# Optimization experiments

Hardware: AMD Instinct MI355X
Metric: run time of the kernel (lower is better)

Reference implementation:

```python
import jax, jax.numpy as jnp
import numpy as np

IN_F, OUT_F, RANK = 4096, 4096, 16
SCALING = 1.0  # alpha defaults to rank -> alpha/rank == 1.0


def setup_inputs() -> dict:
    key = jax.random.key(0)
    k1, k2, k3, k4 = jax.random.split(key, 4)
    x = jax.random.normal(k1, (4, 2048, IN_F), dtype=jnp.float32)
    base_weight = jax.random.normal(k2, (OUT_F, IN_F), dtype=jnp.float32)
    U = jax.random.normal(k3, (OUT_F, RANK), dtype=jnp.float32)
    s = jnp.ones((RANK,), dtype=jnp.float32)
    V = jax.random.normal(k4, (IN_F, RANK), dtype=jnp.float32)
    return {"x": x, "base_weight": base_weight, "U": U, "s": s, "V": V}


def reference(x, base_weight, U, s, V):
    # delta_weight = scaling * (U * s) @ V^T, shape (out, in)
    delta_w = SCALING * jnp.einsum('or,ir->oi', U * s[None, :], V)
    adapted = base_weight + delta_w
    # x @ adapted^T : (..., in) -> (..., out)
    return jnp.einsum('bsi,oi->bso', x, adapted)
```

## Files before the change

### kernel.cpp

```cpp
#include <hip/hip_runtime.h>


#define IN_F   4096
#define OUT_F  4096
#define RANK   16
#define M_ROWS 8192
#define BM 256
#define BN 256
#define BK 64
#define NT (IN_F / BK)

typedef _Float16 f16x8 __attribute__((ext_vector_type(8)));
typedef _Float16 f16x4 __attribute__((ext_vector_type(4)));
typedef float    f32x4 __attribute__((ext_vector_type(4)));

__device__ __forceinline__ void async16(const void* gp, void* lp) {
  __builtin_amdgcn_global_load_lds(
      (const __attribute__((address_space(1))) void*)gp,
      (__attribute__((address_space(3))) void*)lp, 16, 0, 0);
}

#define SPLIT_BLOCKS 4096

__global__ __launch_bounds__(256)
void prep_kernel(const float* __restrict__ x, _Float16* __restrict__ xh,
                 const float* __restrict__ W, const float* __restrict__ U,
                 const float* __restrict__ S, const float* __restrict__ V,
                 _Float16* __restrict__ wh) {
  if (blockIdx.x < SPLIT_BLOCKS) {
    size_t t = (size_t)blockIdx.x * 256 + threadIdx.x;
#pragma unroll
    for (int it = 0; it < 8; ++it) {
      float4 v = ((const float4*)x)[t];
      f16x4 h;
      h[0] = (_Float16)v.x; h[1] = (_Float16)v.y;
      h[2] = (_Float16)v.z; h[3] = (_Float16)v.w;
      ((f16x4*)xh)[t] = h;
      t += (size_t)SPLIT_BLOCKS * 256;
    }
  } else {
    int t = (int)(blockIdx.x - SPLIT_BLOCKS) * 256 + threadIdx.x;
    int i4 = (t & 1023) << 2;
    int o0 = (t >> 10) << 3;

    float v[4][RANK];
#pragma unroll
    for (int j = 0; j < 4; ++j) {
      const float4* vp = (const float4*)(V + (size_t)(i4 + j) * RANK);
#pragma unroll
      for (int q = 0; q < 4; ++q) {
        float4 vv = vp[q];
        v[j][q * 4 + 0] = vv.x; v[j][q * 4 + 1] = vv.y;
        v[j][q * 4 + 2] = vv.z; v[j][q * 4 + 3] = vv.w;
      }
    }
    float sv[RANK];
#pragma unroll
    for (int r = 0; r < RANK; r += 4) {
      float4 ss = *(const float4*)(S + r);
      sv[r] = ss.x; sv[r + 1] = ss.y; sv[r + 2] = ss.z; sv[r + 3] = ss.w;
    }

    for (int oo = 0; oo < 8; ++oo) {
      int o = o0 + oo;
      float us[RANK];
      const float4* up = (const float4*)(U + (size_t)o * RANK);
#pragma unroll
      for (int r = 0; r < RANK; r += 4) {
        float4 uu = up[r >> 2];
        us[r] = uu.x * sv[r]; us[r + 1] = uu.y * sv[r + 1];
        us[r + 2] = uu.z * sv[r + 2]; us[r + 3] = uu.w * sv[r + 3];
      }
      float4 w = *(const float4*)(W + (size_t)o * IN_F + i4);
      float d0 = w.x, d1 = w.y, d2 = w.z, d3 = w.w;
#pragma unroll
      for (int r = 0; r < RANK; ++r) {
        d0 += us[r] * v[0][r];
        d1 += us[r] * v[1][r];
        d2 += us[r] * v[2][r];
        d3 += us[r] * v[3][r];
      }
      f16x4 h;
      h[0] = (_Float16)d0; h[1] = (_Float16)d1;
      h[2] = (_Float16)d2; h[3] = (_Float16)d3;
      *(f16x4*)(wh + (size_t)o * IN_F + i4) = h;
    }
  }
}

__global__ __launch_bounds__(512, 2)
void gemm_kernel(const _Float16* __restrict__ xh,
                 const _Float16* __restrict__ wh,
                 float* __restrict__ out) {
  __shared__ unsigned char lds[131072];

  const int orig = blockIdx.x;
  const int wg = (orig & 7) * 64 + (orig >> 3);
  const int mt = wg >> 4;
  const int nt = wg & 15;
  const int blockM = mt * BM;
  const int blockN = nt * BN;

  const int tid = threadIdx.x;
  const int lane = tid & 63;
  const int wave = tid >> 6;
  const int wm = wave >> 2;
  const int wn = wave & 3;

  const _Float16* aSrc[2];
  const _Float16* bSrc[2];
  unsigned ldsOff[2];
#pragma unroll
  for (int q = 0; q < 2; ++q) {
    int slot = q * 512 + tid;
    int r = slot >> 2;
    int c = slot & 3;
    int cd = c ^ ((r >> 1) & 3);
    aSrc[q] = xh + (size_t)(blockM + r) * IN_F + cd * 8;
    bSrc[q] = wh + (size_t)(blockN + r) * IN_F + cd * 8;
    ldsOff[q] = (unsigned)slot * 16;
  }

  const int kg = lane >> 4;
  unsigned offA[4], offB[4];
#pragma unroll
  for (int t = 0; t < 4; ++t) {
    int ar = wm * 128 + t * 16 + (lane & 15);
    offA[t] = (unsigned)(ar * 64 + ((kg ^ ((ar >> 1) & 3)) * 16));
    int br = wn * 64 + t * 16 + (lane & 15);
    offB[t] = (unsigned)(br * 64 + ((kg ^ ((br >> 1) & 3)) * 16));
  }

  f32x4 acc[8][4];
#pragma unroll
  for (int i = 0; i < 8; ++i)
#pragma unroll
    for (int j = 0; j < 4; ++j) acc[i][j] = (f32x4){0.f, 0.f, 0.f, 0.f};

  f16x8 aFA[4], aFB[4], bF0[4], bF1[4];

#define STG(SRC, LDSBASE, KOFS)                                      \
  {                                                                  \
    async16(SRC[0] + (KOFS), lds + (LDSBASE) + ldsOff[0]);           \
    async16(SRC[1] + (KOFS), lds + (LDSBASE) + ldsOff[1]);           \
  }
#define RD4(DST, RB, OFF)                                            \
  {                                                                  \
    DST[0] = *(const f16x8*)(lds + (RB) + OFF[0]);                   \
    DST[1] = *(const f16x8*)(lds + (RB) + OFF[1]);                   \
    DST[2] = *(const f16x8*)(lds + (RB) + OFF[2]);                   \
    DST[3] = *(const f16x8*)(lds + (RB) + OFF[3]);                   \
  }
#define PH_BAR() asm volatile("s_barrier" ::: "memory")
#define WAITL(N) asm volatile("s_waitcnt lgkmcnt(" #N ")" ::: "memory")
#define WAITV(N) asm volatile("s_waitcnt vmcnt(" #N ")" ::: "memory")
#define MFMA16(AO, A, B)                                             \
  {                                                                  \
    __builtin_amdgcn_sched_barrier(0);                               \
    __builtin_amdgcn_s_setprio(1);                                   \
    _Pragma("unroll")                                                \
    for (int i_ = 0; i_ < 4; ++i_) {                                 \
      _Pragma("unroll")                                              \
      for (int j_ = 0; j_ < 4; ++j_)                                 \
        acc[(AO) + i_][j_] = __builtin_amdgcn_mfma_f32_16x16x32_f16( \
            (A)[i_], (B)[j_], acc[(AO) + i_][j_], 0, 0, 0);          \
    }                                                                \
    __builtin_amdgcn_s_setprio(0);                                   \
  }

  STG(aSrc, 0, 0);
  STG(bSrc, 16384, 0);
  STG(aSrc, 32768, 32);
  STG(bSrc, 49152, 32);
  STG(bSrc, 65536 + 16384, 64);
  STG(aSrc, 65536 + 0, 64);
  STG(bSrc, 65536 + 49152, 96);
  WAITV(6);
  PH_BAR();
  RD4(aFA, 0, offA);
  RD4(bF0, 16384, offB);

#pragma unroll 2
  for (int t = 0; t < NT - 2; ++t) {
    const unsigned base  = (unsigned)(t & 1) << 16;
    const unsigned baseN = base ^ 65536u;
    const int kof1 = (t + 1) * BK;
    const int kof2 = (t + 2) * BK;

    PH_BAR();
    RD4(aFB, base + 4096, offA);
    STG(aSrc, baseN + 32768, kof1 + 32);
    WAITL(4);
    MFMA16(0, aFA, bF0);

    PH_BAR();
    RD4(aFA, base + 32768, offA);
    RD4(bF1, base + 49152, offB);
    STG(bSrc, base + 16384, kof2);
    WAITL(8);
    MFMA16(4, aFB, bF0);

    PH_BAR();
    RD4(aFB, base + 32768 + 4096, offA);
    STG(aSrc, base + 0, kof2);
    WAITL(4);
    MFMA16(0, aFA, bF1);

    WAITV(4);
    PH_BAR();
    RD4(aFA, baseN + 0, offA);
    RD4(bF0, baseN + 16384, offB);
    STG(bSrc, base + 49152, kof2 + 32);
    WAITL(8);
    MFMA16(4, aFB, bF1);
  }

  {
    const unsigned base = 0, baseN = 65536u;
    const int kof1 = (NT - 1) * BK;
    PH_BAR();
    RD4(aFB, base + 4096, offA);
    STG(aSrc, baseN + 32768, kof1 + 32);
    WAITL(4);
    MFMA16(0, aFA, bF0);

    PH_BAR();
    RD4(aFA, base + 32768, offA);
    RD4(bF1, base + 49152, offB);
    WAITL(8);
    MFMA16(4, aFB, bF0);

    PH_BAR();
    RD4(aFB, base + 32768 + 4096, offA);
    WAITL(4);
    MFMA16(0, aFA, bF1);

    WAITV(0);
    PH_BAR();
    RD4(aFA, baseN + 0, offA);
    RD4(bF0, baseN + 16384, offB);
    WAITL(8);
    MFMA16(4, aFB, bF1);
  }
  {
    const unsigned base = 65536u;
    PH_BAR();
    RD4(aFB, base + 4096, offA);
    WAITL(4);
    MFMA16(0, aFA, bF0);

    PH_BAR();
    RD4(aFA, base + 32768, offA);
    RD4(bF1, base + 49152, offB);
    WAITL(8);
    MFMA16(4, aFB, bF0);

    PH_BAR();
    RD4(aFB, base + 32768 + 4096, offA);
    WAITL(4);
    MFMA16(0, aFA, bF1);

    PH_BAR();
    WAITL(0);
    MFMA16(4, aFB, bF1);
  }
#undef STG
#undef RD4
#undef PH_BAR
#undef WAITL
#undef WAITV
#undef MFMA16

  const int col0 = blockN + wn * 64 + (lane & 15);
  const int row0 = blockM + wm * 128 + (lane >> 4) * 4;
#pragma unroll
  for (int i = 0; i < 8; ++i)
#pragma unroll
    for (int j = 0; j < 4; ++j) {
      float* op = out + (size_t)(row0 + i * 16) * OUT_F + col0 + j * 16;
#pragma unroll
      for (int rr = 0; rr < 4; ++rr) op[(size_t)rr * OUT_F] = acc[i][j][rr];
    }
}

__global__ __launch_bounds__(256)
void fb_gemm(const float* __restrict__ x, const float* __restrict__ W,
             float* __restrict__ out) {
  __shared__ float xs[64][17];
  __shared__ float wsm[64][17];
  const int mt = blockIdx.x >> 6;
  const int ntile = blockIdx.x & 63;
  const int bM = mt * 64, bN = ntile * 64;
  const int t = threadIdx.x;
  const int lr = t >> 2, lc = (t & 3) * 4;
  const int tm = t >> 4, tn = t & 15;

  float acc[4][4];
#pragma unroll
  for (int i = 0; i < 4; ++i)
#pragma unroll
    for (int j = 0; j < 4; ++j) acc[i][j] = 0.f;

  for (int kk = 0; kk < IN_F; kk += 16) {
    float4 xa = *(const float4*)(x + (size_t)(bM + lr) * IN_F + kk + lc);
    float4 wa = *(const float4*)(W + (size_t)(bN + lr) * IN_F + kk + lc);
    xs[lr][lc + 0] = xa.x; xs[lr][lc + 1] = xa.y;
    xs[lr][lc + 2] = xa.z; xs[lr][lc + 3] = xa.w;
    wsm[lr][lc + 0] = wa.x; wsm[lr][lc + 1] = wa.y;
    wsm[lr][lc + 2] = wa.z; wsm[lr][lc + 3] = wa.w;
    __syncthreads();
#pragma unroll
    for (int k = 0; k < 16; ++k) {
      float a[4], b[4];
#pragma unroll
      for (int i = 0; i < 4; ++i) a[i] = xs[tm * 4 + i][k];
#pragma unroll
      for (int j = 0; j < 4; ++j) b[j] = wsm[tn * 4 + j][k];
#pragma unroll
      for (int i = 0; i < 4; ++i)
#pragma unroll
        for (int j = 0; j < 4; ++j) acc[i][j] += a[i] * b[j];
    }
    __syncthreads();
  }
#pragma unroll
  for (int i = 0; i < 4; ++i)
#pragma unroll
    for (int j = 0; j < 4; ++j)
      out[(size_t)(bM + tm * 4 + i) * OUT_F + bN + tn * 4 + j] = acc[i][j];
}

__global__ void fb_xv(const float* __restrict__ x, const float* __restrict__ V,
                      const float* __restrict__ S, float* __restrict__ xv) {
  int m = blockIdx.x * 4 + (threadIdx.x >> 6);
  int lane = threadIdx.x & 63;
  float a[RANK];
#pragma unroll
  for (int r = 0; r < RANK; ++r) a[r] = 0.f;
  for (int k = lane; k < IN_F; k += 64) {
    float xe = x[(size_t)m * IN_F + k];
    const float4* vp = (const float4*)(V + (size_t)k * RANK);
#pragma unroll
    for (int q = 0; q < 4; ++q) {
      float4 vv = vp[q];
      a[q * 4 + 0] += xe * vv.x; a[q * 4 + 1] += xe * vv.y;
      a[q * 4 + 2] += xe * vv.z; a[q * 4 + 3] += xe * vv.w;
    }
  }
#pragma unroll
  for (int r = 0; r < RANK; ++r)
    for (int off = 32; off; off >>= 1) a[r] += __shfl_down(a[r], off);
  if (lane == 0) {
#pragma unroll
    for (int r = 0; r < RANK; ++r) xv[(size_t)m * RANK + r] = a[r] * S[r];
  }
}

__global__ void fb_add(const float* __restrict__ xv, const float* __restrict__ U,
                       float* __restrict__ out) {
  size_t t = (size_t)blockIdx.x * 256 + threadIdx.x;
  int m = (int)(t >> 12), o = (int)(t & 4095);
  const float* xr = xv + (size_t)m * RANK;
  const float* ur = U + (size_t)o * RANK;
  float d = 0.f;
#pragma unroll
  for (int r = 0; r < RANK; ++r) d += xr[r] * ur[r];
  out[t] += d;
}

extern "C" void kernel_launch(void* const* d_in, const int* in_sizes, int n_in,
                              void* d_out, int out_size, void* d_ws, size_t ws_size,
                              hipStream_t stream) {
  const float* x = (const float*)d_in[0];
  const float* W = (const float*)d_in[1];
  const float* U = (const float*)d_in[2];
  const float* s = (const float*)d_in[3];
  const float* V = (const float*)d_in[4];
  float* out = (float*)d_out;

  const size_t need = ((size_t)M_ROWS * IN_F + (size_t)OUT_F * IN_F) * 2;
  if (ws_size >= need) {
    _Float16* xh = (_Float16*)d_ws;
    _Float16* wh = xh + (size_t)M_ROWS * IN_F;
    prep_kernel<<<SPLIT_BLOCKS + ((IN_F / 4) * (OUT_F / 8)) / 256, 256, 0, stream>>>(
        x, xh, W, U, s, V, wh);
    gemm_kernel<<<(M_ROWS / BM) * (OUT_F / BN), 512, 0, stream>>>(xh, wh, out);
  } else {
    float* xv = (float*)d_ws;
    fb_gemm<<<(M_ROWS / 64) * (OUT_F / 64), 256, 0, stream>>>(x, W, out);
    fb_xv<<<M_ROWS / 4, 256, 0, stream>>>(x, V, s, xv);
    fb_add<<<(size_t)M_ROWS * OUT_F / 256, 256, 0, stream>>>(xv, U, out);
  }
}
```

Before: 537.9 us.

## Switch main GEMM to 32x32x16 MFMA tiles and widen fp16 conversion stores

Replaces the 16x16x32 MFMA inner tiling with 32x32x16 MFMA instructions. This changes the per-lane LDS fragment offsets, the accumulator layout (f32x16), the LDS read schedule and wait counts, the staging order, and the output write mapping. Larger MFMA tiles reduce LDS fragment reads per FLOP and the instruction count. The prep kernel also converts x with 8-wide fp16 stores instead of 4-wide. The trade-off is reworked pipeline wait counts, which risk hazards or stalls, and a less coalesced epilogue store pattern.

Result: no change. 538.5 us (+0.1%).

```diff
diff --git a/kernel.cpp b/kernel.cpp
--- a/kernel.cpp
+++ b/kernel.cpp
@@ -13,6 +13,7 @@
 typedef _Float16 f16x8 __attribute__((ext_vector_type(8)));
 typedef _Float16 f16x4 __attribute__((ext_vector_type(4)));
 typedef float    f32x4 __attribute__((ext_vector_type(4)));
+typedef float    f32x16 __attribute__((ext_vector_type(16)));
 
 __device__ __forceinline__ void async16(const void* gp, void* lp) {
   __builtin_amdgcn_global_load_lds(
@@ -29,13 +30,17 @@
                  _Float16* __restrict__ wh) {
   if (blockIdx.x < SPLIT_BLOCKS) {
     size_t t = (size_t)blockIdx.x * 256 + threadIdx.x;
-#pragma unroll
-    for (int it = 0; it < 8; ++it) {
-      float4 v = ((const float4*)x)[t];
-      f16x4 h;
-      h[0] = (_Float16)v.x; h[1] = (_Float16)v.y;
-      h[2] = (_Float16)v.z; h[3] = (_Float16)v.w;
-      ((f16x4*)xh)[t] = h;
+    const float4* xin = (const float4*)x;
+#pragma unroll
+    for (int it = 0; it < 4; ++it) {
+      float4 a = xin[2 * t];
+      float4 b = xin[2 * t + 1];
+      f16x8 h;
+      h[0] = (_Float16)a.x; h[1] = (_Float16)a.y;
+      h[2] = (_Float16)a.z; h[3] = (_Float16)a.w;
+      h[4] = (_Float16)b.x; h[5] = (_Float16)b.y;
+      h[6] = (_Float16)b.z; h[7] = (_Float16)b.w;
+      ((f16x8*)xh)[t] = h;
       t += (size_t)SPLIT_BLOCKS * 256;
     }
   } else {
@@ -121,49 +126,59 @@
     ldsOff[q] = (unsigned)slot * 16;
   }
 
-  const int kg = lane >> 4;
-  unsigned offA[4], offB[4];
-#pragma unroll
-  for (int t = 0; t < 4; ++t) {
-    int ar = wm * 128 + t * 16 + (lane & 15);
-    offA[t] = (unsigned)(ar * 64 + ((kg ^ ((ar >> 1) & 3)) * 16));
-    int br = wn * 64 + t * 16 + (lane & 15);
-    offB[t] = (unsigned)(br * 64 + ((kg ^ ((br >> 1) & 3)) * 16));
-  }
-
-  f32x4 acc[8][4];
-#pragma unroll
-  for (int i = 0; i < 8; ++i)
-#pragma unroll
-    for (int j = 0; j < 4; ++j) acc[i][j] = (f32x4){0.f, 0.f, 0.f, 0.f};
-
-  f16x8 aFA[4], aFB[4], bF0[4], bF1[4];
+  const int kg = lane >> 5;
+  const int lr = lane & 31;
+  unsigned offA32[4][2], offB32[2][2];
+#pragma unroll
+  for (int rt = 0; rt < 4; ++rt) {
+    int ar = wm * 128 + rt * 32 + lr;
+    int sw = (ar >> 1) & 3;
+    offA32[rt][0] = (unsigned)(ar * 64 + (((0 * 2 + kg) ^ sw) * 16));
+    offA32[rt][1] = (unsigned)(ar * 64 + (((1 * 2 + kg) ^ sw) * 16));
+  }
+#pragma unroll
+  for (int ct = 0; ct < 2; ++ct) {
+    int br = wn * 64 + ct * 32 + lr;
+    int sw = (br >> 1) & 3;
+    offB32[ct][0] = (unsigned)(br * 64 + (((0 * 2 + kg) ^ sw) * 16));
+    offB32[ct][1] = (unsigned)(br * 64 + (((1 * 2 + kg) ^ sw) * 16));
+  }
+
+  f32x16 acc[4][2];
+#pragma unroll
+  for (int i = 0; i < 4; ++i)
+#pragma unroll
+    for (int j = 0; j < 2; ++j) acc[i][j] = (f32x16)(0.f);
+
+  f16x8 a0[4], b0[2], a1[4], b1[2];
 
 #define STG(SRC, LDSBASE, KOFS)                                      \
   {                                                                  \
     async16(SRC[0] + (KOFS), lds + (LDSBASE) + ldsOff[0]);           \
     async16(SRC[1] + (KOFS), lds + (LDSBASE) + ldsOff[1]);           \
   }
-#define RD4(DST, RB, OFF)                                            \
+#define RD6(AA, BB, RA, RB, SL)                                      \
   {                                                                  \
-    DST[0] = *(const f16x8*)(lds + (RB) + OFF[0]);                   \
-    DST[1] = *(const f16x8*)(lds + (RB) + OFF[1]);                   \
-    DST[2] = *(const f16x8*)(lds + (RB) + OFF[2]);                   \
-    DST[3] = *(const f16x8*)(lds + (RB) + OFF[3]);                   \
+    AA[0] = *(const f16x8*)(lds + (RA) + offA32[0][SL]);             \
+    AA[1] = *(const f16x8*)(lds + (RA) + offA32[1][SL]);             \
+    AA[2] = *(const f16x8*)(lds + (RA) + offA32[2][SL]);             \
+    AA[3] = *(const f16x8*)(lds + (RA) + offA32[3][SL]);             \
+    BB[0] = *(const f16x8*)(lds + (RB) + offB32[0][SL]);             \
+    BB[1] = *(const f16x8*)(lds + (RB) + offB32[1][SL]);             \
   }
 #define PH_BAR() asm volatile("s_barrier" ::: "memory")
 #define WAITL(N) asm volatile("s_waitcnt lgkmcnt(" #N ")" ::: "memory")
 #define WAITV(N) asm volatile("s_waitcnt vmcnt(" #N ")" ::: "memory")
-#define MFMA16(AO, A, B)                                             \
+#define MFMA8(AA, BB)                                                \
   {                                                                  \
     __builtin_amdgcn_sched_barrier(0);                               \
     __builtin_amdgcn_s_setprio(1);                                   \
     _Pragma("unroll")                                                \
-    for (int i_ = 0; i_ < 4; ++i_) {                                 \
+    for (int rt_ = 0; rt_ < 4; ++rt_) {                              \
       _Pragma("unroll")                                              \
-      for (int j_ = 0; j_ < 4; ++j_)                                 \
-        acc[(AO) + i_][j_] = __builtin_amdgcn_mfma_f32_16x16x32_f16( \
-            (A)[i_], (B)[j_], acc[(AO) + i_][j_], 0, 0, 0);          \
+      for (int ct_ = 0; ct_ < 2; ++ct_)                              \
+        acc[rt_][ct_] = __builtin_amdgcn_mfma_f32_32x32x16_f16(      \
+            (AA)[rt_], (BB)[ct_], acc[rt_][ct_], 0, 0, 0);           \
     }                                                                \
     __builtin_amdgcn_s_setprio(0);                                   \
   }
@@ -172,13 +187,11 @@
   STG(bSrc, 16384, 0);
   STG(aSrc, 32768, 32);
   STG(bSrc, 49152, 32);
+  STG(aSrc, 65536 + 0, 64);
   STG(bSrc, 65536 + 16384, 64);
-  STG(aSrc, 65536 + 0, 64);
-  STG(bSrc, 65536 + 49152, 96);
-  WAITV(6);
+  WAITV(8);
   PH_BAR();
-  RD4(aFA, 0, offA);
-  RD4(bF0, 16384, offB);
+  RD6(a0, b0, 0, 16384, 0);
 
 #pragma unroll 2
   for (int t = 0; t < NT - 2; ++t) {
@@ -188,98 +201,102 @@
     const int kof2 = (t + 2) * BK;
 
     PH_BAR();
-    RD4(aFB, base + 4096, offA);
+    RD6(a1, b1, base + 0, base + 16384, 1);
     STG(aSrc, baseN + 32768, kof1 + 32);
-    WAITL(4);
-    MFMA16(0, aFA, bF0);
-
-    PH_BAR();
-    RD4(aFA, base + 32768, offA);
-    RD4(bF1, base + 49152, offB);
+    WAITL(6);
+    MFMA8(a0, b0);
+
+    WAITV(6);
+    PH_BAR();
+    RD6(a0, b0, base + 32768, base + 49152, 0);
+    STG(bSrc, baseN + 49152, kof1 + 32);
+    WAITL(6);
+    MFMA8(a1, b1);
+
+    PH_BAR();
+    RD6(a1, b1, base + 32768, base + 49152, 1);
+    STG(aSrc, base + 0, kof2);
+    WAITL(6);
+    MFMA8(a0, b0);
+
+    WAITV(6);
+    PH_BAR();
+    RD6(a0, b0, baseN + 0, baseN + 16384, 0);
     STG(bSrc, base + 16384, kof2);
-    WAITL(8);
-    MFMA16(4, aFB, bF0);
-
-    PH_BAR();
-    RD4(aFB, base + 32768 + 4096, offA);
-    STG(aSrc, base + 0, kof2);
-    WAITL(4);
-    MFMA16(0, aFA, bF1);
-
-    WAITV(4);
-    PH_BAR();
-    RD4(aFA, baseN + 0, offA);
-    RD4(bF0, baseN + 16384, offB);
-    STG(bSrc, base + 49152, kof2 + 32);
-    WAITL(8);
-    MFMA16(4, aFB, bF1);
+    WAITL(6);
+    MFMA8(a1, b1);
   }
 
   {
     const unsigned base = 0, baseN = 65536u;
     const int kof1 = (NT - 1) * BK;
-    PH_BAR();
-    RD4(aFB, base + 4096, offA);
+
+    PH_BAR();
+    RD6(a1, b1, base + 0, base + 16384, 1);
     STG(aSrc, baseN + 32768, kof1 + 32);
-    WAITL(4);
-    MFMA16(0, aFA, bF0);
-
-    PH_BAR();
-    RD4(aFA, base + 32768, offA);
-    RD4(bF1, base + 49152, offB);
-    WAITL(8);
-    MFMA16(4, aFB, bF0);
-
-    PH_BAR();
-    RD4(aFB, base + 32768 + 4096, offA);
-    WAITL(4);
-    MFMA16(0, aFA, bF1);
-
-    WAITV(0);
-    PH_BAR();
-    RD4(aFA, baseN + 0, offA);
-    RD4(bF0, baseN + 16384, offB);
-    WAITL(8);
-    MFMA16(4, aFB, bF1);
+    WAITL(6);
+    MFMA8(a0, b0);
+
+    WAITV(6);
+    PH_BAR();
+    RD6(a0, b0, base + 32768, base + 49152, 0);
+    STG(bSrc, baseN + 49152, kof1 + 32);
+    WAITL(6);
+    MFMA8(a1, b1);
+
+    PH_BAR();
+    RD6(a1, b1, base + 32768, base + 49152, 1);
+    WAITL(6);
+    MFMA8(a0, b0);
+
+    WAITV(4);
+    PH_BAR();
+    RD6(a0, b0, baseN + 0, baseN + 16384, 0);
+    WAITL(6);
+    MFMA8(a1, b1);
   }
   {
     const unsigned base = 65536u;
-    PH_BAR();
-    RD4(aFB, base + 4096, offA);
-    WAITL(4);
-    MFMA16(0, aFA, bF0);
-
-    PH_BAR();
-    RD4(aFA, base + 32768, offA);
-    RD4(bF1, base + 49152, offB);
-    WAITL(8);
-    MFMA16(4, aFB, bF0);
-
-    PH_BAR();
-    RD4(aFB, base + 32768 + 4096, offA);
-    WAITL(4);
-    MFMA16(0, aFA, bF1);
+
+    PH_BAR();
+    RD6(a1, b1, base + 0, base + 16384, 1);
+    WAITL(6);
+    MFMA8(a0, b0);
+
+    WAITV(0);
+    PH_BAR();
+    RD6(a0, b0, base + 32768, base + 49152, 0);
+    WAITL(6);
+    MFMA8(a1, b1);
+
+    PH_BAR();
+    RD6(a1, b1, base + 32768, base + 49152, 1);
+    WAITL(6);
+    MFMA8(a0, b0);
 
     PH_BAR();
     WAITL(0);
-    MFMA16(4, aFB, bF1);
+    MFMA8(a1, b1);
   }
 #undef STG
-#undef RD4
+#undef RD6
 #undef PH_BAR
 #undef WAITL
 #undef WAITV
-#undef MFMA16
-
-  const int col0 = blockN + wn * 64 + (lane & 15);
-  const int row0 = blockM + wm * 128 + (lane >> 4) * 4;
-#pragma unroll
-  for (int i = 0; i < 8; ++i)
-#pragma unroll
-    for (int j = 0; j < 4; ++j) {
-      float* op = out + (size_t)(row0 + i * 16) * OUT_F + col0 + j * 16;
-#pragma unroll
-      for (int rr = 0; rr < 4; ++rr) op[(size_t)rr * OUT_F] = acc[i][j][rr];
+#undef MFMA8
+
+  const int colB = blockN + wn * 64 + lr;
+  const int rowB = blockM + wm * 128 + 4 * kg;
+#pragma unroll
+  for (int rt = 0; rt < 4; ++rt)
+#pragma unroll
+    for (int ct = 0; ct < 2; ++ct) {
+#pragma unroll
+      for (int g = 0; g < 4; ++g)
+#pragma unroll
+        for (int q = 0; q < 4; ++q)
+          out[(size_t)(rowB + rt * 32 + 8 * g + q) * OUT_F + colB + ct * 32] =
+              acc[rt][ct][g * 4 + q];
     }
 }
 
```
